# Performance work log

Measured on AMD Instinct MI355X. Metric: run time of the kernel, lower is better.

Reference implementation:

```python
import jax, jax.numpy as jnp
import numpy as np

B, A, D, H = 32, 64, 128, 512
F = A * D  # 8192

def setup_inputs() -> dict:
    key = jax.random.key(0)
    ks = jax.random.split(key, 20)
    s = 0.02
    return {
        "swarm_states": jax.random.normal(ks[0], (B, A, D), jnp.float32),
        "swarm_goals": jax.random.normal(ks[1], (B, A, D), jnp.float32),
        # quantum layer stand-in: Linear(F->F) + tanh
        "Wq": jax.random.normal(ks[2], (F, F), jnp.float32) * s,
        "bq": jnp.zeros((F,), jnp.float32),
        # interaction_net: Linear(2D->H) ReLU Linear(H->H) ReLU Linear(H->D)
        "Wi1": jax.random.normal(ks[3], (2 * D, H), jnp.float32) * s,
        "bi1": jnp.zeros((H,), jnp.float32),
        "Wi2": jax.random.normal(ks[4], (H, H), jnp.float32) * s,
        "bi2": jnp.zeros((H,), jnp.float32),
        "Wi3": jax.random.normal(ks[5], (H, D), jnp.float32) * s,
        "bi3": jnp.zeros((D,), jnp.float32),
        # coordination_net: Linear(F->H) ReLU Linear(H->H) ReLU Linear(H->F)
        "Wc1": jax.random.normal(ks[6], (F, H), jnp.float32) * s,
        "bc1": jnp.zeros((H,), jnp.float32),
        "Wc2": jax.random.normal(ks[7], (H, H), jnp.float32) * s,
        "bc2": jnp.zeros((H,), jnp.float32),
        "Wc3": jax.random.normal(ks[8], (H, F), jnp.float32) * s,
        "bc3": jnp.zeros((F,), jnp.float32),
    }

def reference(swarm_states, swarm_goals, Wq, bq, Wi1, bi1, Wi2, bi2, Wi3, bi3,
              Wc1, bc1, Wc2, bc2, Wc3, bc3):
    b, a, d = swarm_states.shape
    states_flat = swarm_states.reshape(b, a * d)
    # quantum feature extraction (stand-in for QuantumNeuralLayer)
    quantum_features = jnp.tanh(states_flat @ Wq + bq)  # (B, A*D)

    # vectorized pairwise interaction MLP over all ordered (i, j) pairs
    xi = jnp.broadcast_to(swarm_states[:, :, None, :], (b, a, a, d))
    xj = jnp.broadcast_to(swarm_states[:, None, :, :], (b, a, a, d))
    pair = jnp.concatenate([xi, xj], axis=-1)            # (B, A, A, 2D)
    h = jax.nn.relu(pair @ Wi1 + bi1)
    h = jax.nn.relu(h @ Wi2 + bi2)
    inter = h @ Wi3 + bi3                                # (B, A, A, D)
    offdiag = (1.0 - jnp.eye(a, dtype=inter.dtype))[None, :, :, None]
    # per-agent aggregation over the other agents (mean over j != i)
    interactions = (inter * offdiag).sum(axis=2) / (a - 1)  # (B, A, D)

    c = jax.nn.relu(quantum_features @ Wc1 + bc1)
    c = jax.nn.relu(c @ Wc2 + bc2)
    coordination = (c @ Wc3 + bc3).reshape(b, a, d)      # (B, A, D)

    coordinated_states = swarm_states + 0.1 * interactions + 0.1 * coordination
    return coordinated_states, quantum_features, interactions, coordination
```

## Files before the change

kernel.cpp:

```cpp
#include <hip/hip_runtime.h>

typedef __attribute__((ext_vector_type(8))) short bf16x8;
typedef __attribute__((ext_vector_type(16))) float f32x16;
typedef _Float16 f16;
typedef __attribute__((ext_vector_type(8))) _Float16 f16x8;

static __device__ __forceinline__ unsigned short f2bf(float x) {
  unsigned int u = __float_as_uint(x);
  return (unsigned short)((u + 0x7FFFu + ((u >> 16) & 1u)) >> 16);
}
static __device__ __forceinline__ unsigned int pk2bf(float lo, float hi) {
  return ((unsigned int)f2bf(hi) << 16) | f2bf(lo);
}
static __device__ __forceinline__ f16x8 relu8(f16x8 x) {
  f16x8 z = {0, 0, 0, 0, 0, 0, 0, 0};
  return __builtin_elementwise_max(x, z);
}

__global__ __launch_bounds__(256) void prep_kernel(const float* __restrict__ states,
                                                   const float* __restrict__ Wi2,
                                                   const float* __restrict__ Wi1,
                                                   const float* __restrict__ bi1,
                                                   unsigned short* __restrict__ Sbf,
                                                   f16* __restrict__ W2h,
                                                   f16* __restrict__ Uh, f16* __restrict__ Vh) {
  __shared__ float lds_f[1536];
  const int t = threadIdx.x;
  const int bid = blockIdx.x;
  if (bid < 256) {
    const int idx = bid * 256 + t;
    float4 v = ((const float4*)states)[idx];
    ushort4 o;
    o.x = f2bf(v.x); o.y = f2bf(v.y); o.z = f2bf(v.z); o.w = f2bf(v.w);
    ((ushort4*)Sbf)[idx] = o;
  } else if (bid < 512) {
    const int b = bid - 256;
    const int bk = b & 15, bn = b >> 4;
    float (*tile)[33] = (float(*)[33])lds_f;
    const int r = t >> 5, c = t & 31;
#pragma unroll
    for (int p = 0; p < 4; p++) {
      int rr = p * 8 + r;
      tile[rr][c] = Wi2[(bk * 32 + rr) * 512 + bn * 32 + c];
    }
    __syncthreads();
#pragma unroll
    for (int p = 0; p < 4; p++) {
      int rr = p * 8 + r;
      W2h[(bn * 32 + rr) * 512 + bk * 32 + c] = (f16)tile[c][rr];
    }
  } else {
    const int row0 = (bid - 512) * 8;
    float (*st)[12] = (float(*)[12])lds_f;
    for (int idx = t; idx < 1024; idx += 256) {
      int r = idx >> 7, k = idx & 127;
      st[k][r] = states[(row0 + r) * 128 + k];
    }
    __syncthreads();
    float au0[8], au1[8], av0[8], av1[8];
#pragma unroll
    for (int r = 0; r < 8; r++) { au0[r] = 0.f; au1[r] = 0.f; av0[r] = 0.f; av1[r] = 0.f; }
#pragma unroll 4
    for (int k = 0; k < 128; k++) {
      float wt0 = Wi1[k * 512 + t];
      float wt1 = Wi1[k * 512 + 256 + t];
      float wb0 = Wi1[(k + 128) * 512 + t];
      float wb1 = Wi1[(k + 128) * 512 + 256 + t];
      float4 sA = *(const float4*)&st[k][0];
      float4 sB = *(const float4*)&st[k][4];
      float s8[8] = {sA.x, sA.y, sA.z, sA.w, sB.x, sB.y, sB.z, sB.w};
#pragma unroll
      for (int r = 0; r < 8; r++) {
        au0[r] += s8[r] * wt0;
        au1[r] += s8[r] * wt1;
        av0[r] += s8[r] * wb0;
        av1[r] += s8[r] * wb1;
      }
    }
    const float b0 = bi1[t], b1 = bi1[256 + t];
#pragma unroll
    for (int r = 0; r < 8; r++) {
      Uh[(row0 + r) * 512 + t]       = (f16)(au0[r] + b0);
      Uh[(row0 + r) * 512 + 256 + t] = (f16)(au1[r] + b1);
      Vh[(row0 + r) * 512 + t]       = (f16)av0[r];
      Vh[(row0 + r) * 512 + 256 + t] = (f16)av1[r];
    }
  }
}

__global__ __launch_bounds__(256, 4) void gemmw3(const unsigned short* __restrict__ Abf,
                                                 const float* __restrict__ W,
                                                 float* __restrict__ P,
                                                 int K, int N) {
  __shared__ __align__(16) unsigned short As[32 * 512];
  __shared__ __align__(16) char Bs[8192];
  const int t = threadIdx.x;
  const int k0 = blockIdx.y * 512;
  for (int idx = t; idx < 4096; idx += 256) {
    int row = idx >> 7, k4 = idx & 127;
    ushort4 a4 = *(const ushort4*)&Abf[(size_t)row * K + k0 + k4 * 4];
    int off = (row * 1024 + k4 * 8) ^ ((row & 7) << 4);
    *(ushort4*)((char*)As + off) = a4;
  }

  const int lane = t & 63, w = t >> 6;
  const int lrow = lane & 31, lh = lane >> 5;
  const int c0 = blockIdx.x * 128;
  const int srow = t >> 5;
  const int sc4 = t & 31;
  const float* Wst = W + (size_t)k0 * N + c0 + sc4 * 4;

  const int nr = w * 32 + lrow;
  const int bread = lh * 2048 + ((nr * 16) ^ (((nr >> 3) & 7) << 4));
  const int abase = lrow * 1024 + lh * 16;
  const int aswz = (lrow & 7) << 4;

  f32x16 acc;
#pragma unroll
  for (int r = 0; r < 16; r++) acc[r] = 0.f;

  float4 r0, r1;
  r0 = *(const float4*)&Wst[(size_t)(srow) * N];
  r1 = *(const float4*)&Wst[(size_t)(srow + 8) * N];
  __syncthreads();

  for (int ks = 0; ks < 32; ks++) {
    char* bb = Bs + (ks & 1) * 4096;
    {
      int lh0 = srow >> 3, j0 = srow & 7;
      int lh1 = (srow + 8) >> 3, j1 = srow & 7;
      float v0[4] = {r0.x, r0.y, r0.z, r0.w};
      float v1[4] = {r1.x, r1.y, r1.z, r1.w};
#pragma unroll
      for (int cc = 0; cc < 4; cc++) {
        int n = sc4 * 4 + cc;
        int sl = (n * 16) ^ (((n >> 3) & 7) << 4);
        *(unsigned short*)(bb + lh0 * 2048 + sl + j0 * 2) = f2bf(v0[cc]);
        *(unsigned short*)(bb + lh1 * 2048 + sl + j1 * 2) = f2bf(v1[cc]);
      }
    }
    __syncthreads();
    if (ks < 31) {
      r0 = *(const float4*)&Wst[(size_t)((ks + 1) * 16 + srow) * N];
      r1 = *(const float4*)&Wst[(size_t)((ks + 1) * 16 + srow + 8) * N];
    }
    bf16x8 af = *(const bf16x8*)((const char*)As + ((abase + ks * 32) ^ aswz));
    bf16x8 bf = *(const bf16x8*)(Bs + (ks & 1) * 4096 + bread);
    acc = __builtin_amdgcn_mfma_f32_32x32x16_bf16(af, bf, acc, 0, 0, 0);
  }

  float* Pr = P + (size_t)blockIdx.y * 32 * N + c0 + nr;
#pragma unroll
  for (int r = 0; r < 16; r++) {
    int row = (r & 3) + 8 * (r >> 2) + 4 * lh;
    Pr[(size_t)row * N] = acc[r];
  }
}

__global__ __launch_bounds__(256, 5) void gemmw(const unsigned short* __restrict__ Abf,
                                                const float* __restrict__ W,
                                                float* __restrict__ P,
                                                int K, int N, int L, int l4sh) {
  __shared__ __align__(16) unsigned short As[32 * 512];
  const int t = threadIdx.x;
  const int k0 = blockIdx.y * L;
  const int L4 = L >> 2;
  const int swzm = 2 * L - 1;
  for (int idx = t; idx < (L << 3); idx += 256) {
    int row = idx >> l4sh, k4 = idx & (L4 - 1);
    ushort4 a4 = *(const ushort4*)&Abf[(size_t)row * K + k0 + k4 * 4];
    int off = (row * 2 * L + k4 * 8) ^ (((row & 7) << 4) & swzm);
    *(ushort4*)((char*)As + off) = a4;
  }
  __syncthreads();
  const int lane = t & 63, w = t >> 6;
  const int lrow = lane & 31, lh = lane >> 5;
  const int col = blockIdx.x * 128 + w * 32 + lrow;
  f32x16 acc0, acc1;
#pragma unroll
  for (int r = 0; r < 16; r++) { acc0[r] = 0.f; acc1[r] = 0.f; }
  const float* Wp = W + (size_t)(k0 + lh * 8) * N + col;
  const int aswz = ((lrow & 7) << 4) & swzm;
  const int abase = lrow * 2 * L + lh * 16;
  const int nks = L >> 4;
  int ks = 0;
  for (; ks + 1 < nks; ks += 2) {
    float wv0[8], wv1[8];
#pragma unroll
    for (int jj = 0; jj < 8; jj++) wv0[jj] = Wp[(size_t)(ks * 16 + jj) * N];
#pragma unroll
    for (int jj = 0; jj < 8; jj++) wv1[jj] = Wp[(size_t)(ks * 16 + 16 + jj) * N];
    uint4 b0, b1;
    b0.x = pk2bf(wv0[0], wv0[1]); b0.y = pk2bf(wv0[2], wv0[3]);
    b0.z = pk2bf(wv0[4], wv0[5]); b0.w = pk2bf(wv0[6], wv0[7]);
    b1.x = pk2bf(wv1[0], wv1[1]); b1.y = pk2bf(wv1[2], wv1[3]);
    b1.z = pk2bf(wv1[4], wv1[5]); b1.w = pk2bf(wv1[6], wv1[7]);
    bf16x8 af0 = *(const bf16x8*)((const char*)As + ((abase + ks * 32) ^ aswz));
    bf16x8 af1 = *(const bf16x8*)((const char*)As + ((abase + ks * 32 + 32) ^ aswz));
    acc0 = __builtin_amdgcn_mfma_f32_32x32x16_bf16(af0, *(const bf16x8*)&b0, acc0, 0, 0, 0);
    acc1 = __builtin_amdgcn_mfma_f32_32x32x16_bf16(af1, *(const bf16x8*)&b1, acc1, 0, 0, 0);
  }
  if (ks < nks) {
    float wv0[8];
#pragma unroll
    for (int jj = 0; jj < 8; jj++) wv0[jj] = Wp[(size_t)(ks * 16 + jj) * N];
    uint4 b0;
    b0.x = pk2bf(wv0[0], wv0[1]); b0.y = pk2bf(wv0[2], wv0[3]);
    b0.z = pk2bf(wv0[4], wv0[5]); b0.w = pk2bf(wv0[6], wv0[7]);
    bf16x8 af0 = *(const bf16x8*)((const char*)As + ((abase + ks * 32) ^ aswz));
    acc0 = __builtin_amdgcn_mfma_f32_32x32x16_bf16(af0, *(const bf16x8*)&b0, acc0, 0, 0, 0);
  }
  float* Pr = P + (size_t)blockIdx.y * 32 * N + col;
#pragma unroll
  for (int r = 0; r < 16; r++) {
    int row = (r & 3) + 8 * (r >> 2) + 4 * lh;
    Pr[(size_t)row * N] = acc0[r] + acc1[r];
  }
}

__global__ __launch_bounds__(256) void reduce_kernel(const float* __restrict__ P,
                                                     const float* __restrict__ bias,
                                                     float* __restrict__ dst,
                                                     unsigned short* __restrict__ dstbf,
                                                     int lnN, int KS, int act, int wbf,
                                                     const float* __restrict__ S,
                                                     const float* __restrict__ Ip,
                                                     float* __restrict__ out0, int comb) {
  const int idx = blockIdx.x * 256 + threadIdx.x;
  const int N = 1 << lnN;
  const int m = idx >> lnN, n = idx & (N - 1);
  float s = 0.f;
#pragma unroll 8
  for (int p = 0; p < KS; p++) s += P[((size_t)(p * 32 + m) << lnN) + n];
  s += bias[n];
  if (act == 1) s = fmaxf(s, 0.f);
  else if (act == 2) s = tanhf(s);
  dst[idx] = s;
  if (wbf) dstbf[idx] = f2bf(s);
  if (comb) out0[idx] = S[idx] + 0.1f * (Ip[idx] + s);
}

__global__ __launch_bounds__(512, 2) void inter6_kernel(const f16* __restrict__ Uh,
                                                        const f16* __restrict__ Vh,
                                                        const f16* __restrict__ W2h,
                                                        const float* __restrict__ bi2,
                                                        float* __restrict__ Hsum) {
  __shared__ __align__(16) f16 Bt[128 * 512];
  __shared__ __align__(16) f16 Vc[64 * 128];
  const int t = threadIdx.x;
  const int nq = blockIdx.x;

#pragma unroll
  for (int i = 0; i < 16; i++) {
    int idx = i * 512 + t;
    int n = idx >> 6, ch = idx & 63;
    f16x8 w8 = *(const f16x8*)&W2h[(size_t)(nq * 128 + n) * 512 + ch * 8];
    int off = (n * 1024 + ch * 16) ^ ((n & 15) << 4);
    *(f16x8*)((char*)Bt + off) = w8;
  }

  const int w = t >> 6, lane = t & 63;
  const int ii = w & 1, tg = w >> 1;
  const int lrow = lane & 31, lh = lane >> 5;
  const char* Btc = (const char*)Bt;
  const char* Vcc = (const char*)Vc;
  char* Vcw = (char*)Vc;

  int bofs[4], bswz[4];
#pragma unroll
  for (int nf = 0; nf < 4; nf++) {
    int nr = nf * 32 + lrow;
    bofs[nf] = nr * 1024 + lh * 16;
    bswz[nf] = (nr & 15) << 4;
  }
  const int vofs0 = lrow * 256;
  const int vswz0 = (lrow & 15) << 4;
  const int vofs1 = (lrow + 32) * 256;
  const int vswz1 = vswz0;

  const int b = blockIdx.y >> 1;

  for (int s = 0; s < 4; s++) {
    const int tid = blockIdx.y * 16 + tg * 4 + s;
    const int it = tid & 31;
    const f16* Ub = Uh + (size_t)(b * 64 + it * 2 + ii) * 512 + lh * 8;

    f32x16 acc[2][4];
#pragma unroll
    for (int mf = 0; mf < 2; mf++)
#pragma unroll
      for (int nf = 0; nf < 4; nf++)
#pragma unroll
        for (int r = 0; r < 16; r++) acc[mf][nf][r] = 0.f;

    for (int ch = 0; ch < 4; ch++) {
      const int kc = ch * 128;
      __syncthreads();
#pragma unroll
      for (int i = 0; i < 2; i++) {
        int idx = i * 512 + t;
        int row = idx >> 4, c8 = idx & 15;
        f16x8 w8 = *(const f16x8*)&Vh[(size_t)(b * 64 + row) * 512 + kc + c8 * 8];
        *(f16x8*)(Vcw + ((row * 256 + c8 * 16) ^ ((row & 15) << 4))) = w8;
      }
      __syncthreads();
#pragma unroll
      for (int k16 = 0; k16 < 8; k16++) {
        const int kb2 = k16 * 32 + lh * 16;
        f16x8 v0 = *(const f16x8*)(Vcc + ((vofs0 + kb2) ^ vswz0));
        f16x8 v1 = *(const f16x8*)(Vcc + ((vofs1 + kb2) ^ vswz1));
        f16x8 u0 = *(const f16x8*)(Ub + kc + k16 * 16);
        f16x8 a0 = relu8(v0 + u0);
        f16x8 a1 = relu8(v1 + u0);
#pragma unroll
        for (int nf = 0; nf < 4; nf++) {
          f16x8 bfr = *(const f16x8*)(Btc + ((bofs[nf] + (kc + k16 * 16) * 2) ^ bswz[nf]));
          acc[0][nf] = __builtin_amdgcn_mfma_f32_32x32x16_f16(a0, bfr, acc[0][nf], 0, 0, 0);
          acc[1][nf] = __builtin_amdgcn_mfma_f32_32x32x16_f16(a1, bfr, acc[1][nf], 0, 0, 0);
        }
      }
    }

    const int iglob = it * 2 + ii;
    const int mf_d = iglob >> 5;
    const int rd = iglob & 31;
    const int lh_d = (rd >> 2) & 1;
    const int r_d = (rd & 3) + 4 * (rd >> 3);
#pragma unroll
    for (int nf = 0; nf < 4; nf++) {
      const int col = nq * 128 + nf * 32 + lrow;
      const float b2 = bi2[col];
      float ssum = 0.f;
#pragma unroll
      for (int mf = 0; mf < 2; mf++)
#pragma unroll
        for (int r = 0; r < 16; r++) {
          float x = fmaxf(acc[mf][nf][r] + b2, 0.f);
          if (mf == mf_d && r == r_d && lh == lh_d) x = 0.f;
          ssum += x;
        }
      ssum += __shfl_xor(ssum, 32);
      if (lh == 0) Hsum[(size_t)(b * 64 + iglob) * 512 + col] = ssum;
    }
  }
}

__global__ __launch_bounds__(256) void k3_kernel(const float* __restrict__ Hsum,
                                                 const float* __restrict__ Wi3,
                                                 const float* __restrict__ bi3,
                                                 float* __restrict__ inter) {
  __shared__ float st[512][10];
  const int t = threadIdx.x;
  const int row0 = blockIdx.x * 8;
  for (int idx = t; idx < 4096; idx += 256) {
    int r = idx >> 9, k = idx & 511;
    st[k][r] = Hsum[(row0 + r) * 512 + k] * (1.0f / 63.0f);
  }
  __syncthreads();
  const int c = t & 63;
  const int rg = t >> 6;
  float a0[2] = {0.f, 0.f}, a1[2] = {0.f, 0.f};
#pragma unroll 4
  for (int k = 0; k < 512; k++) {
    float w0 = Wi3[k * 128 + c];
    float w1 = Wi3[k * 128 + 64 + c];
    float2 h = *(const float2*)&st[k][rg * 2];
    a0[0] += h.x * w0; a0[1] += h.y * w0;
    a1[0] += h.x * w1; a1[1] += h.y * w1;
  }
  float b0 = bi3[c], b1 = bi3[64 + c];
#pragma unroll
  for (int r = 0; r < 2; r++) {
    inter[(row0 + rg * 2 + r) * 128 + c]      = a0[r] + b0;
    inter[(row0 + rg * 2 + r) * 128 + 64 + c] = a1[r] + b1;
  }
}

extern "C" void kernel_launch(void* const* d_in, const int* in_sizes, int n_in,
                              void* d_out, int out_size, void* d_ws, size_t ws_size,
                              hipStream_t stream) {
  const float* states = (const float*)d_in[0];
  const float* Wq  = (const float*)d_in[2];
  const float* bq  = (const float*)d_in[3];
  const float* Wi1 = (const float*)d_in[4];
  const float* bi1 = (const float*)d_in[5];
  const float* Wi2 = (const float*)d_in[6];
  const float* bi2 = (const float*)d_in[7];
  const float* Wi3 = (const float*)d_in[8];
  const float* bi3 = (const float*)d_in[9];
  const float* Wc1 = (const float*)d_in[10];
  const float* bc1 = (const float*)d_in[11];
  const float* Wc2 = (const float*)d_in[12];
  const float* bc2 = (const float*)d_in[13];
  const float* Wc3 = (const float*)d_in[14];
  const float* bc3 = (const float*)d_in[15];

  float* out   = (float*)d_out;
  float* out0  = out;
  float* qf    = out + 262144;
  float* inter = out + 524288;
  float* coord = out + 786432;

  char* ws = (char*)d_ws;
  float*          P    = (float*)(ws);
  f16*            Uh   = (f16*)(ws + ((size_t)16 << 20));
  f16*            Vh   = (f16*)(ws + ((size_t)19 << 20));
  f16*            W2h  = (f16*)(ws + ((size_t)22 << 20));
  float*          Hsum = (float*)(ws + ((size_t)23 << 20));
  unsigned short* Sbf  = (unsigned short*)(ws + ((size_t)27 << 20));
  unsigned short* qfbf = (unsigned short*)(ws + ((size_t)28 << 20));
  float*          c1   = (float*)(ws + ((size_t)29 << 20));
  float*          c2   = (float*)(ws + ((size_t)29 << 20) + (1 << 16));
  unsigned short* c1bf = (unsigned short*)(ws + ((size_t)29 << 20) + (2 << 16));
  unsigned short* c2bf = (unsigned short*)(ws + ((size_t)29 << 20) + (3 << 16));

  prep_kernel<<<768, 256, 0, stream>>>(states, Wi2, Wi1, bi1, Sbf, W2h, Uh, Vh);

  gemmw3<<<dim3(64, 16), 256, 0, stream>>>(Sbf, Wq, P, 8192, 8192);
  reduce_kernel<<<1024, 256, 0, stream>>>(P, bq, qf, qfbf, 13, 16, 2, 1,
                                          nullptr, nullptr, nullptr, 0);

  inter6_kernel<<<dim3(4, 64), 512, 0, stream>>>(Uh, Vh, W2h, bi2, Hsum);
  k3_kernel<<<256, 256, 0, stream>>>(Hsum, Wi3, bi3, inter);

  gemmw<<<dim3(4, 64), 256, 0, stream>>>(qfbf, Wc1, P, 8192, 512, 128, 5);
  reduce_kernel<<<64, 256, 0, stream>>>(P, bc1, c1, c1bf, 9, 64, 1, 1,
                                        nullptr, nullptr, nullptr, 0);
  gemmw<<<dim3(4, 32), 256, 0, stream>>>(c1bf, Wc2, P, 512, 512, 16, 2);
  reduce_kernel<<<64, 256, 0, stream>>>(P, bc2, c2, c2bf, 9, 32, 1, 1,
                                        nullptr, nullptr, nullptr, 0);

  gemmw<<<dim3(64, 8), 256, 0, stream>>>(c2bf, Wc3, P, 512, 8192, 64, 4);
  reduce_kernel<<<1024, 256, 0, stream>>>(P, bc3, coord, nullptr, 13, 8, 0, 0,
                                          states, inter, out0, 1);
}
```

Measured before the change: 217.3 us.

## Halve interaction kernel N-tile and stage full V tile in LDS once

The pairwise-interaction kernel now covers 64 output columns per block instead of 128, and the grid doubles to 8x64 blocks. With the smaller weight tile, the whole 64x512 V slice fits in LDS and is loaded once up front. This removes the per-K-chunk reload of V and the two barriers around each chunk. The trade-off is that each block reuses the A fragments (relu(U+V)) across fewer MFMAs, so that elementwise work is repeated across more blocks, and launch bounds drop to one block per CU.

```diff
diff --git a/kernel.cpp b/kernel.cpp
--- a/kernel.cpp
+++ b/kernel.cpp
@@ -240,84 +240,73 @@
   if (comb) out0[idx] = S[idx] + 0.1f * (Ip[idx] + s);
 }
 
-__global__ __launch_bounds__(512, 2) void inter6_kernel(const f16* __restrict__ Uh,
+__global__ __launch_bounds__(512, 1) void inter9_kernel(const f16* __restrict__ Uh,
                                                         const f16* __restrict__ Vh,
                                                         const f16* __restrict__ W2h,
                                                         const float* __restrict__ bi2,
                                                         float* __restrict__ Hsum) {
-  __shared__ __align__(16) f16 Bt[128 * 512];
-  __shared__ __align__(16) f16 Vc[64 * 128];
+  __shared__ __align__(16) f16 Bt[64 * 512];
+  __shared__ __align__(16) f16 Vc[64 * 512];
   const int t = threadIdx.x;
   const int nq = blockIdx.x;
-
-#pragma unroll
-  for (int i = 0; i < 16; i++) {
+  const int b = blockIdx.y >> 1;
+
+#pragma unroll
+  for (int i = 0; i < 8; i++) {
     int idx = i * 512 + t;
     int n = idx >> 6, ch = idx & 63;
-    f16x8 w8 = *(const f16x8*)&W2h[(size_t)(nq * 128 + n) * 512 + ch * 8];
+    f16x8 w8 = *(const f16x8*)&W2h[(size_t)(nq * 64 + n) * 512 + ch * 8];
     int off = (n * 1024 + ch * 16) ^ ((n & 15) << 4);
     *(f16x8*)((char*)Bt + off) = w8;
-  }
+    f16x8 v8 = *(const f16x8*)&Vh[(size_t)(b * 64 + n) * 512 + ch * 8];
+    *(f16x8*)((char*)Vc + off) = v8;
+  }
+  __syncthreads();
 
   const int w = t >> 6, lane = t & 63;
   const int ii = w & 1, tg = w >> 1;
   const int lrow = lane & 31, lh = lane >> 5;
   const char* Btc = (const char*)Bt;
   const char* Vcc = (const char*)Vc;
-  char* Vcw = (char*)Vc;
-
-  int bofs[4], bswz[4];
-#pragma unroll
-  for (int nf = 0; nf < 4; nf++) {
+
+  int bofs[2], bswz[2];
+#pragma unroll
+  for (int nf = 0; nf < 2; nf++) {
     int nr = nf * 32 + lrow;
     bofs[nf] = nr * 1024 + lh * 16;
     bswz[nf] = (nr & 15) << 4;
   }
-  const int vofs0 = lrow * 256;
+  const int vofs0 = lrow * 1024 + lh * 16;
   const int vswz0 = (lrow & 15) << 4;
-  const int vofs1 = (lrow + 32) * 256;
+  const int vofs1 = (lrow + 32) * 1024 + lh * 16;
   const int vswz1 = vswz0;
-
-  const int b = blockIdx.y >> 1;
 
   for (int s = 0; s < 4; s++) {
     const int tid = blockIdx.y * 16 + tg * 4 + s;
     const int it = tid & 31;
     const f16* Ub = Uh + (size_t)(b * 64 + it * 2 + ii) * 512 + lh * 8;
 
-    f32x16 acc[2][4];
+    f32x16 acc[2][2];
 #pragma unroll
     for (int mf = 0; mf < 2; mf++)
 #pragma unroll
-      for (int nf = 0; nf < 4; nf++)
+      for (int nf = 0; nf < 2; nf++)
 #pragma unroll
         for (int r = 0; r < 16; r++) acc[mf][nf][r] = 0.f;
 
-    for (int ch = 0; ch < 4; ch++) {
-      const int kc = ch * 128;
-      __syncthreads();
-#pragma unroll
-      for (int i = 0; i < 2; i++) {
-        int idx = i * 512 + t;
-        int row = idx >> 4, c8 = idx & 15;
-        f16x8 w8 = *(const f16x8*)&Vh[(size_t)(b * 64 + row) * 512 + kc + c8 * 8];
-        *(f16x8*)(Vcw + ((row * 256 + c8 * 16) ^ ((row & 15) << 4))) = w8;
-      }
-      __syncthreads();
-#pragma unroll
-      for (int k16 = 0; k16 < 8; k16++) {
-        const int kb2 = k16 * 32 + lh * 16;
-        f16x8 v0 = *(const f16x8*)(Vcc + ((vofs0 + kb2) ^ vswz0));
-        f16x8 v1 = *(const f16x8*)(Vcc + ((vofs1 + kb2) ^ vswz1));
-        f16x8 u0 = *(const f16x8*)(Ub + kc + k16 * 16);
-        f16x8 a0 = relu8(v0 + u0);
-        f16x8 a1 = relu8(v1 + u0);
-#pragma unroll
-        for (int nf = 0; nf < 4; nf++) {
-          f16x8 bfr = *(const f16x8*)(Btc + ((bofs[nf] + (kc + k16 * 16) * 2) ^ bswz[nf]));
-          acc[0][nf] = __builtin_amdgcn_mfma_f32_32x32x16_f16(a0, bfr, acc[0][nf], 0, 0, 0);
-          acc[1][nf] = __builtin_amdgcn_mfma_f32_32x32x16_f16(a1, bfr, acc[1][nf], 0, 0, 0);
-        }
+#pragma unroll 4
+    for (int k16 = 0; k16 < 32; k16++) {
+      const int kb = k16 * 32;
+      f16x8 v0 = *(const f16x8*)(Vcc + ((vofs0 + kb) ^ vswz0));
+      f16x8 v1 = *(const f16x8*)(Vcc + ((vofs1 + kb) ^ vswz1));
+      f16x8 u0 = *(const f16x8*)(Ub + k16 * 16);
+      f16x8 a0 = relu8(v0 + u0);
+      f16x8 a1 = relu8(v1 + u0);
+#pragma unroll
+      for (int nf = 0; nf < 2; nf++) {
+        f16x8 bfr = *(const f16x8*)(Btc + ((bofs[nf] + kb) ^ bswz[nf]));
+        acc[0][nf] = __builtin_amdgcn_mfma_f32_32x32x16_f16(a0, bfr, acc[0][nf], 0, 0, 0);
+        acc[1][nf] = __builtin_amdgcn_mfma_f32_32x32x16_f16(a1, bfr, acc[1][nf], 0, 0, 0);
       }
     }
 
@@ -327,8 +316,8 @@
     const int lh_d = (rd >> 2) & 1;
     const int r_d = (rd & 3) + 4 * (rd >> 3);
 #pragma unroll
-    for (int nf = 0; nf < 4; nf++) {
-      const int col = nq * 128 + nf * 32 + lrow;
+    for (int nf = 0; nf < 2; nf++) {
+      const int col = nq * 64 + nf * 32 + lrow;
       const float b2 = bi2[col];
       float ssum = 0.f;
 #pragma unroll
@@ -420,7 +409,7 @@
   reduce_kernel<<<1024, 256, 0, stream>>>(P, bq, qf, qfbf, 13, 16, 2, 1,
                                           nullptr, nullptr, nullptr, 0);
 
-  inter6_kernel<<<dim3(4, 64), 512, 0, stream>>>(Uh, Vh, W2h, bi2, Hsum);
+  inter9_kernel<<<dim3(8, 64), 512, 0, stream>>>(Uh, Vh, W2h, bi2, Hsum);
   k3_kernel<<<256, 256, 0, stream>>>(Hsum, Wi3, bi3, inter);
 
   gemmw<<<dim3(4, 64), 256, 0, stream>>>(qfbf, Wc1, P, 8192, 512, 128, 5);
```

Result: slower. 227.2 us (+4.5%).
